# Optimization experiments

Hardware: AMD Instinct MI355X
Metric: run time of the kernel (lower is better)

Reference implementation:

```python
import jax, jax.numpy as jnp
import numpy as np

NUM_VISUAL = 16
MAX_PATCH = 1024
DIM = 1280
NUM_HEADS = 16
HEAD_DIM = DIM // NUM_HEADS  # 80


def _make_rope_cache(key):
    # cos/sin cache per (visual, patch): (N, P, 1, head_dim*2) = [cos | sin]
    inv_freq = 1.0 / (10000.0 ** (jnp.arange(0, HEAD_DIM, 2, dtype=jnp.float32) / HEAD_DIM))  # (hd/2,)
    pos = jnp.arange(MAX_PATCH, dtype=jnp.float32)  # (P,)
    freqs = pos[:, None] * inv_freq[None, :]              # (P, hd/2)
    emb = jnp.concatenate([freqs, freqs], axis=-1)        # (P, hd)
    cos = jnp.cos(emb)
    sin = jnp.sin(emb)
    cache = jnp.concatenate([cos, sin], axis=-1)          # (P, 2*hd)
    return jnp.broadcast_to(cache[None, :, None, :], (NUM_VISUAL, MAX_PATCH, 1, 2 * HEAD_DIM))


def setup_inputs() -> dict:
    key = jax.random.key(0)
    k1, k2, k3, k4, k5, k6 = jax.random.split(key, 6)
    s = 0.02
    hidden_states = jax.random.normal(k1, (NUM_VISUAL, MAX_PATCH, DIM), dtype=jnp.float32)
    rope_cache = _make_rope_cache(k2)
    seq_lens = jax.random.randint(k3, (NUM_VISUAL,), 512, MAX_PATCH + 1, dtype=jnp.int32)
    w_qkv = jax.random.normal(k4, (3 * DIM, DIM), dtype=jnp.float32) * s
    b_qkv = jnp.zeros((3 * DIM,), dtype=jnp.float32)
    w_proj = jax.random.normal(k5, (DIM, DIM), dtype=jnp.float32) * s
    b_proj = jnp.zeros((DIM,), dtype=jnp.float32)
    return {"hidden_states": hidden_states, "rope_cache": rope_cache, "seq_lens": seq_lens,
            "w_qkv": w_qkv, "b_qkv": b_qkv, "w_proj": w_proj, "b_proj": b_proj}


def _rotate_half(x):
    x1, x2 = jnp.split(x, 2, axis=-1)
    return jnp.concatenate([-x2, x1], axis=-1)


def reference(hidden_states, rope_cache, seq_lens, w_qkv, b_qkv, w_proj, b_proj):
    N, P, D = hidden_states.shape
    H, hd = NUM_HEADS, HEAD_DIM
    # QKV projection: (N, P, 3D) -> (N, P, 3, H, hd)
    qkv = (hidden_states @ w_qkv.T + b_qkv).reshape(N, P, 3, H, hd)
    q, k, v = qkv[:, :, 0], qkv[:, :, 1], qkv[:, :, 2]  # each (N, P, H, hd)
    # RoPE via precomputed cos/sin: rope_cache (N, P, 1, 2*hd)
    cos = rope_cache[..., :hd]   # (N, P, 1, hd), broadcasts over heads
    sin = rope_cache[..., hd:]
    q = q * cos + _rotate_half(q) * sin
    k = k * cos + _rotate_half(k) * sin
    # Attention with key-padding mask (BlockMask equivalent for varlen patches)
    scale = 1.0 / jnp.sqrt(jnp.asarray(hd, dtype=q.dtype))
    scores = jnp.einsum("nqhd,nkhd->nhqk", q, k) * scale  # (N, H, P, P)
    key_valid = jnp.arange(P, dtype=jnp.int32)[None, :] < seq_lens[:, None]  # (N, P)
    neg = jnp.asarray(-1e30, dtype=scores.dtype)
    scores = jnp.where(key_valid[:, None, None, :], scores, neg)
    attn = jax.nn.softmax(scores, axis=-1)
    out = jnp.einsum("nhqk,nkhd->nqhd", attn, v).reshape(N, P, D)
    return out @ w_proj.T + b_proj
```

## Files before the change

### kernel.cpp

```cpp
#include <hip/hip_runtime.h>
#include <stdint.h>

#define DIM     1280
#define NHEADS  16
#define HD      80
#define NV      16
#define MAXP    1024
#define MTOT    (NV*MAXP)

typedef __bf16 bf16;
using bf16x8 = __attribute__((ext_vector_type(8))) __bf16;
using bf16x4 = __attribute__((ext_vector_type(4))) __bf16;
using f32x4  = __attribute__((ext_vector_type(4))) float;

#define GLOAD_LDS16(g, l)                                                     \
    __builtin_amdgcn_global_load_lds(                                         \
        (const __attribute__((address_space(1))) void*)(g),                   \
        (__attribute__((address_space(3))) void*)(l), 16, 0, 0)

__global__ __launch_bounds__(256)
void cvt_bf16(const float* __restrict__ src, bf16* __restrict__ dst, int n4)
{
    const int i = blockIdx.x * 256 + threadIdx.x;
    if (i < n4) {
        const float4 f = ((const float4*)src)[i];
        bf16x4 r;
        r[0] = (bf16)f.x; r[1] = (bf16)f.y; r[2] = (bf16)f.z; r[3] = (bf16)f.w;
        ((bf16x4*)dst)[i] = r;
    }
}

template<bool IS_QKV, int NB, int G>
__global__ __launch_bounds__(256)
void gemm_nt_big(const bf16* __restrict__ A, const bf16* __restrict__ B,
                 const float* __restrict__ bias,
                 bf16* __restrict__ out0, bf16* __restrict__ out1,
                 bf16* __restrict__ out2, float* __restrict__ outf)
{
    const int K = DIM;
    __shared__ __align__(16) bf16 SH[2*128*64];
    bf16* const As = SH;
    bf16* const Bs = SH + 128*64;

    const int tid  = threadIdx.x;
    const int lane = tid & 63, wave = tid >> 6;
    const int quad = lane >> 4, c16 = lane & 15;
    const int wm = wave & 1, wn = wave >> 1;

    const int bid = blockIdx.x;
    const int xcd = bid & 7;
    const int idx = bid >> 3;
    const int nbg = idx / (16*G);
    const int rem = idx % (16*G);
    const int mb  = xcd*16 + rem / G;
    const int nb  = nbg*G  + rem % G;

    const int sr   = lane >> 3;
    const int slot = lane & 7;
    const int sc   = (slot ^ sr) * 8;
    const long a_row0 = (long)mb * 128;
    const long b_row0 = (long)nb * 128;

    const bf16* ga[4];
    const bf16* gb[4];
    #pragma unroll
    for (int c = 0; c < 4; ++c) {
        const int seg = c*4 + wave;
        const int row = seg*8 + sr;
        ga[c] = A + (a_row0 + row)*K + sc;
        gb[c] = B + (b_row0 + row)*K + sc;
    }

    f32x4 acc[4][4] = {};
    const int xr = c16 & 7;

    for (int kt = 0; kt < K/64; ++kt) {
        const int k0 = kt * 64;
        __syncthreads();
        #pragma unroll
        for (int c = 0; c < 4; ++c) {
            const int seg = c*4 + wave;
            GLOAD_LDS16(ga[c] + k0, As + seg*512);
            GLOAD_LDS16(gb[c] + k0, Bs + seg*512);
        }
        __syncthreads();
        #pragma unroll
        for (int kk = 0; kk < 2; ++kk) {
            const int j  = kk*4 + quad;
            const int ko = ((j ^ xr) * 8);
            bf16x8 af[4], bfr[4];
            #pragma unroll
            for (int mt = 0; mt < 4; ++mt)
                af[mt] = *(const bf16x8*)(As + (wm*64 + mt*16 + c16)*64 + ko);
            #pragma unroll
            for (int nt = 0; nt < 4; ++nt)
                bfr[nt] = *(const bf16x8*)(Bs + (wn*64 + nt*16 + c16)*64 + ko);
            #pragma unroll
            for (int mt = 0; mt < 4; ++mt)
                #pragma unroll
                for (int nt = 0; nt < 4; ++nt)
                    acc[mt][nt] = __builtin_amdgcn_mfma_f32_16x16x32_bf16(
                        af[mt], bfr[nt], acc[mt][nt], 0, 0, 0);
        }
    }

    if constexpr (IS_QKV) {
        const int which = nb / 10;
        if (which < 2) {
            bf16* const dst = (which == 0) ? out0 : out1;
            #pragma unroll
            for (int nt = 0; nt < 4; ++nt) {
                const int col = nb*128 + wn*64 + nt*16 + c16;
                const float bv = bias[col];
                const int rr = col - which*DIM;
                const int h  = rr / HD;
                const int d  = rr - h*HD;
                #pragma unroll
                for (int mt = 0; mt < 4; ++mt) {
                    #pragma unroll
                    for (int r = 0; r < 4; ++r) {
                        const int row = mb*128 + wm*64 + mt*16 + quad*4 + r;
                        const int n = row >> 10, p = row & 1023;
                        dst[((long)((n*NHEADS + h)*MAXP + p))*HD + d] =
                            (bf16)(acc[mt][nt][r] + bv);
                    }
                }
            }
        } else {
            __syncthreads();
            #pragma unroll
            for (int nt = 0; nt < 4; ++nt) {
                const int dl0 = wn*64 + nt*16 + c16;
                const float bv = bias[nb*128 + dl0];
                const int swz = (dl0 & 15) << 3;
                #pragma unroll
                for (int mt = 0; mt < 4; ++mt) {
                    #pragma unroll
                    for (int r = 0; r < 4; ++r) {
                        const int pl = wm*64 + mt*16 + quad*4 + r;
                        SH[dl0*128 + (pl ^ swz)] = (bf16)(acc[mt][nt][r] + bv);
                    }
                }
            }
            __syncthreads();
            const int n_    = mb >> 3;
            const int pbase = (mb & 7) * 128;
            #pragma unroll
            for (int it = 0; it < 8; ++it) {
                const int c  = tid + 256*it;
                const int dl = c >> 4, j = c & 15;
                const int p0 = (j ^ (dl & 15)) << 3;
                const int rr = (nb - 20)*128 + dl;
                const int hh = rr / HD;
                const int dd = rr - hh*HD;
                bf16x8 v = *(const bf16x8*)(SH + dl*128 + j*8);
                *(bf16x8*)(out2 + ((long)((n_*NHEADS + hh)*HD + dd))*MAXP
                                  + pbase + p0) = v;
            }
        }
    } else {
        #pragma unroll
        for (int nt = 0; nt < 4; ++nt) {
            const int col = nb*128 + wn*64 + nt*16 + c16;
            const float bv = bias[col];
            #pragma unroll
            for (int mt = 0; mt < 4; ++mt) {
                #pragma unroll
                for (int r = 0; r < 4; ++r) {
                    const int row = mb*128 + wm*64 + mt*16 + quad*4 + r;
                    outf[(long)row*DIM + col] = acc[mt][nt][r] + bv;
                }
            }
        }
    }
}

__global__ __launch_bounds__(320)
void rope_kernel(bf16* __restrict__ qb, bf16* __restrict__ kb,
                 const float* __restrict__ rope)
{
    const int tid = threadIdx.x;
    const int j   = tid % 5;
    const int rl  = tid / 5;
    const long grow = (long)blockIdx.x * 64 + rl;
    const int p = (int)(grow & 1023);
    const int h = (int)((grow >> 10) & 15);
    const int n = (int)((grow >> 14) & 15);
    const int a = (int)(grow >> 18);
    bf16* const arr = a ? kb : qb;
    const long base = ((long)((n*NHEADS + h)*MAXP + p))*HD;
    const float* rc = rope + ((long)(n*MAXP + p))*160;
    const int d = j*8;

    bf16x8 x1v = *(const bf16x8*)(arr + base + d);
    bf16x8 x2v = *(const bf16x8*)(arr + base + 40 + d);

    float c1[8], s1[8], c2[8], s2[8];
    *(float4*)(c1)   = *(const float4*)(rc + d);
    *(float4*)(c1+4) = *(const float4*)(rc + d + 4);
    *(float4*)(s1)   = *(const float4*)(rc + 80 + d);
    *(float4*)(s1+4) = *(const float4*)(rc + 80 + d + 4);
    *(float4*)(c2)   = *(const float4*)(rc + 40 + d);
    *(float4*)(c2+4) = *(const float4*)(rc + 40 + d + 4);
    *(float4*)(s2)   = *(const float4*)(rc + 120 + d);
    *(float4*)(s2+4) = *(const float4*)(rc + 120 + d + 4);

    const float QS = 0.11180339887498949f * 1.4426950408889634f;
    bf16x8 r1, r2;
    #pragma unroll
    for (int i = 0; i < 8; ++i) {
        const float x1 = (float)x1v[i];
        const float x2 = (float)x2v[i];
        float o1 = x1 * c1[i] - x2 * s1[i];
        float o2 = x2 * c2[i] + x1 * s2[i];
        if (a == 0) { o1 *= QS; o2 *= QS; }
        r1[i] = (bf16)o1;
        r2[i] = (bf16)o2;
    }
    *(bf16x8*)(arr + base + d)      = r1;
    *(bf16x8*)(arr + base + 40 + d) = r2;
}

__global__ __launch_bounds__(256)
void attn_kernel(const bf16* __restrict__ qb, const bf16* __restrict__ kb,
                 const bf16* __restrict__ vt, const int* __restrict__ seq_lens,
                 bf16* __restrict__ outb)
{
    __shared__ __align__(16) bf16 Qs[64*104];
    __shared__ __align__(16) bf16 Ks[64*104];
    __shared__ __align__(16) bf16 Vts[80*72];

    const int tid  = threadIdx.x;
    const int lane = tid & 63, wave = tid >> 6;
    const int quad = lane >> 4, c16 = lane & 15;
    const int qt = blockIdx.x, h = blockIdx.y, n = blockIdx.z;
    const int seqlen = seq_lens[n];

    const long qkbase = ((long)(n*NHEADS + h)) * MAXP * HD;
    const long vbase  = ((long)(n*NHEADS + h)) * HD * MAXP;

    const float4 zero4 = make_float4(0.f, 0.f, 0.f, 0.f);

    for (int i = tid; i < 768; i += 256) {
        int row = i / 12, c = i % 12;
        float4 v = (c < 10)
            ? *(const float4*)(qb + qkbase + (long)(qt*64 + row)*HD + c*8)
            : zero4;
        *(float4*)(Qs + row*104 + c*8) = v;
    }
    __syncthreads();
    bf16x8 aq[3];
    #pragma unroll
    for (int kc = 0; kc < 3; ++kc)
        aq[kc] = *(const bf16x8*)(Qs + (wave*16 + c16)*104 + kc*32 + quad*8);

    float mrow = -1e30f, lrow = 0.0f;
    f32x4 O[5] = {};

    union U8 { bf16x8 v; bf16x4 h[2]; };

    const int nkt = (seqlen + 63) >> 6;
    for (int kt = 0; kt < nkt; ++kt) {
        __syncthreads();
        for (int i = tid; i < 768; i += 256) {
            int row = i / 12, c = i % 12;
            float4 v = (c < 10)
                ? *(const float4*)(kb + qkbase + (long)(kt*64 + row)*HD + c*8)
                : zero4;
            *(float4*)(Ks + row*104 + c*8) = v;
        }
        for (int i = tid; i < 640; i += 256) {
            int d = i >> 3, c = i & 7;
            *(float4*)(Vts + d*72 + c*8) =
                *(const float4*)(vt + vbase + (long)d*MAXP + kt*64 + c*8);
        }
        __syncthreads();

        f32x4 S[4] = {};
        #pragma unroll
        for (int kc = 0; kc < 3; ++kc) {
            const int ko = kc*32 + quad*8;
            #pragma unroll
            for (int nt = 0; nt < 4; ++nt) {
                bf16x8 ak = *(const bf16x8*)(Ks + (nt*16 + c16)*104 + ko);
                S[nt] = __builtin_amdgcn_mfma_f32_16x16x32_bf16(ak, aq[kc], S[nt], 0,0,0);
            }
        }
        #pragma unroll
        for (int nt = 0; nt < 4; ++nt) {
            const int key0 = kt*64 + nt*16 + quad*4;
            #pragma unroll
            for (int r = 0; r < 4; ++r)
                if (key0 + r >= seqlen) S[nt][r] = -1e30f;
        }

        float mx[4];
        #pragma unroll
        for (int nt = 0; nt < 4; ++nt)
            mx[nt] = fmaxf(fmaxf(S[nt][0], S[nt][1]), fmaxf(S[nt][2], S[nt][3]));
        float pmax = fmaxf(fmaxf(mx[0], mx[1]), fmaxf(mx[2], mx[3]));
        pmax = fmaxf(pmax, __shfl_xor(pmax, 16));
        pmax = fmaxf(pmax, __shfl_xor(pmax, 32));

        const float nm    = fmaxf(mrow, pmax);
        const float alpha = exp2f(mrow - nm);
        mrow = nm;

        #pragma unroll
        for (int nt = 0; nt < 4; ++nt)
            #pragma unroll
            for (int r = 0; r < 4; ++r)
                S[nt][r] = exp2f(S[nt][r] - nm);

        float sm[4];
        #pragma unroll
        for (int nt = 0; nt < 4; ++nt)
            sm[nt] = (S[nt][0] + S[nt][1]) + (S[nt][2] + S[nt][3]);
        float rs = (sm[0] + sm[1]) + (sm[2] + sm[3]);
        rs += __shfl_xor(rs, 16);
        rs += __shfl_xor(rs, 32);
        lrow = lrow * alpha + rs;

        #pragma unroll
        for (int dt = 0; dt < 5; ++dt)
            #pragma unroll
            for (int r = 0; r < 4; ++r)
                O[dt][r] *= alpha;

        bf16x8 Pk[2];
        #pragma unroll
        for (int nt = 0; nt < 4; ++nt)
            #pragma unroll
            for (int r = 0; r < 4; ++r)
                Pk[nt >> 1][(nt & 1)*4 + r] = (bf16)S[nt][r];

        #pragma unroll
        for (int kc = 0; kc < 2; ++kc) {
            #pragma unroll
            for (int dt = 0; dt < 5; ++dt) {
                U8 av;
                av.h[0] = *(const bf16x4*)(Vts + (dt*16 + c16)*72 + kc*32 + quad*4);
                av.h[1] = *(const bf16x4*)(Vts + (dt*16 + c16)*72 + kc*32 + 16 + quad*4);
                O[dt] = __builtin_amdgcn_mfma_f32_16x16x32_bf16(av.v, Pk[kc], O[dt], 0,0,0);
            }
        }
    }

    const float inv = 1.0f / lrow;
    #pragma unroll
    for (int dt = 0; dt < 5; ++dt)
        #pragma unroll
        for (int r = 0; r < 4; ++r)
            Qs[(wave*16 + c16)*104 + dt*16 + quad*4 + r] = (bf16)(O[dt][r] * inv);
    __syncthreads();
    for (int i = tid; i < 640; i += 256) {
        const int row = i / 10, c = i % 10;
        const float4 v = *(const float4*)(Qs + row*104 + c*8);
        *(float4*)(outb + ((long)(n*MAXP + qt*64 + row))*DIM + h*HD + c*8) = v;
    }
}

extern "C" void kernel_launch(void* const* d_in, const int* in_sizes, int n_in,
                              void* d_out, int out_size, void* d_ws, size_t ws_size,
                              hipStream_t stream)
{
    const float* hidden = (const float*)d_in[0];
    const float* rope   = (const float*)d_in[1];
    const int*   seql   = (const int*)d_in[2];
    const float* wqkv   = (const float*)d_in[3];
    const float* bqkv   = (const float*)d_in[4];
    const float* wproj  = (const float*)d_in[5];
    const float* bproj  = (const float*)d_in[6];
    float* out = (float*)d_out;

    const size_t H_ELEMS  = (size_t)MTOT*DIM;
    const size_t WQ_ELEMS = (size_t)3*DIM*DIM;
    const size_t WP_ELEMS = (size_t)DIM*DIM;
    const size_t QK_ELEMS = (size_t)NV*NHEADS*MAXP*HD;

    bf16* h_bf  = (bf16*)d_ws;
    bf16* wq_bf = h_bf  + H_ELEMS;
    bf16* wp_bf = wq_bf + WQ_ELEMS;

    bf16* q_b = (bf16*)d_out;
    bf16* k_b = q_b + QK_ELEMS;
    bf16* v_t = (bf16*)d_in[0];
    bf16* a_b = v_t + QK_ELEMS;

    cvt_bf16<<<(H_ELEMS/4 + 255)/256, 256, 0, stream>>>(hidden, h_bf, H_ELEMS/4);
    cvt_bf16<<<(WQ_ELEMS/4 + 255)/256, 256, 0, stream>>>(wqkv, wq_bf, WQ_ELEMS/4);
    cvt_bf16<<<(WP_ELEMS/4 + 255)/256, 256, 0, stream>>>(wproj, wp_bf, WP_ELEMS/4);

    gemm_nt_big<true, 30, 6><<<3840, 256, 0, stream>>>(
        h_bf, wq_bf, bqkv, q_b, k_b, v_t, nullptr);

    rope_kernel<<<524288/64, 320, 0, stream>>>(q_b, k_b, rope);

    attn_kernel<<<dim3(MAXP/64, NHEADS, NV), 256, 0, stream>>>(
        q_b, k_b, v_t, seql, a_b);

    gemm_nt_big<false, 10, 10><<<1280, 256, 0, stream>>>(
        a_b, wp_bf, bproj, nullptr, nullptr, nullptr, out);
}
```

Measured before the change: 693.8 us.

## Prefetch next K/V tile into registers and skip unneeded softmax rescales

The attention kernel now issues global loads for the next K and V tile into registers right after the barrier, then writes them to LDS at the start of the following iteration, so load latency overlaps with the current tile's MFMA and softmax work. The key-padding mask is applied only on the last tile. The online-softmax rescale of O and l is skipped when every row's new max stays within 8 of the running max, which cuts the exp and multiply work. MFMA sections are wrapped with s_setprio. The costs are higher register pressure from the prefetch buffers, and with lazy rescaling exp values can reach up to 2^8 before normalization, though this stays within bf16 range.

```diff
diff --git a/kernel.cpp b/kernel.cpp
--- a/kernel.cpp
+++ b/kernel.cpp
@@ -241,6 +241,40 @@
 
     const float4 zero4 = make_float4(0.f, 0.f, 0.f, 0.f);
 
+    int krow[3], kcc[3];
+    #pragma unroll
+    for (int j = 0; j < 3; ++j) {
+        const int i = tid + 256*j;
+        krow[j] = i / 12; kcc[j] = i % 12;
+    }
+    const int vd0 = tid >> 3;
+    const int vd1 = (tid + 256) >> 3;
+    const int vd2 = (tid + 512) >> 3;
+    const int vc  = tid & 7;
+    const bool v2ok = tid < 128;
+
+    float4 kreg[3], vreg[3];
+    auto issue = [&](int ktp) {
+        #pragma unroll
+        for (int j = 0; j < 3; ++j)
+            kreg[j] = (kcc[j] < 10)
+                ? *(const float4*)(kb + qkbase + (long)(ktp*64 + krow[j])*HD + kcc[j]*8)
+                : zero4;
+        vreg[0] = *(const float4*)(vt + vbase + (long)vd0*MAXP + ktp*64 + vc*8);
+        vreg[1] = *(const float4*)(vt + vbase + (long)vd1*MAXP + ktp*64 + vc*8);
+        if (v2ok)
+            vreg[2] = *(const float4*)(vt + vbase + (long)vd2*MAXP + ktp*64 + vc*8);
+    };
+    auto commit = [&]() {
+        #pragma unroll
+        for (int j = 0; j < 3; ++j)
+            *(float4*)(Ks + krow[j]*104 + kcc[j]*8) = kreg[j];
+        *(float4*)(Vts + vd0*72 + vc*8) = vreg[0];
+        *(float4*)(Vts + vd1*72 + vc*8) = vreg[1];
+        if (v2ok) *(float4*)(Vts + vd2*72 + vc*8) = vreg[2];
+    };
+
+    issue(0);
     for (int i = tid; i < 768; i += 256) {
         int row = i / 12, c = i % 12;
         float4 v = (c < 10)
@@ -262,21 +296,12 @@
     const int nkt = (seqlen + 63) >> 6;
     for (int kt = 0; kt < nkt; ++kt) {
         __syncthreads();
-        for (int i = tid; i < 768; i += 256) {
-            int row = i / 12, c = i % 12;
-            float4 v = (c < 10)
-                ? *(const float4*)(kb + qkbase + (long)(kt*64 + row)*HD + c*8)
-                : zero4;
-            *(float4*)(Ks + row*104 + c*8) = v;
-        }
-        for (int i = tid; i < 640; i += 256) {
-            int d = i >> 3, c = i & 7;
-            *(float4*)(Vts + d*72 + c*8) =
-                *(const float4*)(vt + vbase + (long)d*MAXP + kt*64 + c*8);
-        }
+        commit();
         __syncthreads();
+        if (kt + 1 < nkt) issue(kt + 1);
 
         f32x4 S[4] = {};
+        __builtin_amdgcn_s_setprio(1);
         #pragma unroll
         for (int kc = 0; kc < 3; ++kc) {
             const int ko = kc*32 + quad*8;
@@ -286,12 +311,16 @@
                 S[nt] = __builtin_amdgcn_mfma_f32_16x16x32_bf16(ak, aq[kc], S[nt], 0,0,0);
             }
         }
-        #pragma unroll
-        for (int nt = 0; nt < 4; ++nt) {
-            const int key0 = kt*64 + nt*16 + quad*4;
-            #pragma unroll
-            for (int r = 0; r < 4; ++r)
-                if (key0 + r >= seqlen) S[nt][r] = -1e30f;
+        __builtin_amdgcn_s_setprio(0);
+
+        if (kt == nkt - 1) {
+            #pragma unroll
+            for (int nt = 0; nt < 4; ++nt) {
+                const int key0 = kt*64 + nt*16 + quad*4;
+                #pragma unroll
+                for (int r = 0; r < 4; ++r)
+                    if (key0 + r >= seqlen) S[nt][r] = -1e30f;
+            }
         }
 
         float mx[4];
@@ -302,15 +331,23 @@
         pmax = fmaxf(pmax, __shfl_xor(pmax, 16));
         pmax = fmaxf(pmax, __shfl_xor(pmax, 32));
 
-        const float nm    = fmaxf(mrow, pmax);
-        const float alpha = exp2f(mrow - nm);
-        mrow = nm;
+        if (!__all(pmax <= mrow + 8.0f)) {
+            const float nm    = fmaxf(mrow, pmax);
+            const float alpha = exp2f(mrow - nm);
+            mrow = nm;
+            lrow *= alpha;
+            #pragma unroll
+            for (int dt = 0; dt < 5; ++dt)
+                #pragma unroll
+                for (int r = 0; r < 4; ++r)
+                    O[dt][r] *= alpha;
+        }
 
         #pragma unroll
         for (int nt = 0; nt < 4; ++nt)
             #pragma unroll
             for (int r = 0; r < 4; ++r)
-                S[nt][r] = exp2f(S[nt][r] - nm);
+                S[nt][r] = exp2f(S[nt][r] - mrow);
 
         float sm[4];
         #pragma unroll
@@ -319,13 +356,7 @@
         float rs = (sm[0] + sm[1]) + (sm[2] + sm[3]);
         rs += __shfl_xor(rs, 16);
         rs += __shfl_xor(rs, 32);
-        lrow = lrow * alpha + rs;
-
-        #pragma unroll
-        for (int dt = 0; dt < 5; ++dt)
-            #pragma unroll
-            for (int r = 0; r < 4; ++r)
-                O[dt][r] *= alpha;
+        lrow += rs;
 
         bf16x8 Pk[2];
         #pragma unroll
@@ -334,6 +365,7 @@
             for (int r = 0; r < 4; ++r)
                 Pk[nt >> 1][(nt & 1)*4 + r] = (bf16)S[nt][r];
 
+        __builtin_amdgcn_s_setprio(1);
         #pragma unroll
         for (int kc = 0; kc < 2; ++kc) {
             #pragma unroll
@@ -344,6 +376,7 @@
                 O[dt] = __builtin_amdgcn_mfma_f32_16x16x32_bf16(av.v, Pk[kc], O[dt], 0,0,0);
             }
         }
+        __builtin_amdgcn_s_setprio(0);
     }
 
     const float inv = 1.0f / lrow;
```

After: 890.6 us. 1.28x slower.

## Prefetch next K/V tile into registers and add lazy softmax rescaling

Applied to the files above, without the earlier changes.

The attention loop now loads the next K and V tiles from global memory into registers while the current tile is being computed, then writes them to LDS at the start of the next iteration, so global load latency overlaps with MFMA work. The key-padding mask is applied only on the last key tile. The online-softmax rescale of O and l is skipped unless some row's max has grown by more than 8 (log2 units). MFMA sections are also wrapped in s_setprio. This raises register pressure, and lazy rescaling lets exponent values grow up to 2^8 before renormalising.

```diff
diff --git a/kernel.cpp b/kernel.cpp
--- a/kernel.cpp
+++ b/kernel.cpp
@@ -221,6 +221,26 @@
     *(bf16x8*)(arr + base + 40 + d) = r2;
 }
 
+#define ATTN_ISSUE(ktp) do {                                                  \
+    const long kro_ = qkbase + (long)(ktp)*64*HD;                             \
+    kA = k0v ? *(const float4*)(kb + kro_ + (long)kr0*HD + kc0) : zero4;      \
+    kB = k1v ? *(const float4*)(kb + kro_ + (long)kr1*HD + kc1) : zero4;      \
+    kC = k2v ? *(const float4*)(kb + kro_ + (long)kr2*HD + kc2) : zero4;      \
+    const long vro_ = vbase + (long)(ktp)*64 + vc8;                           \
+    vA = *(const float4*)(vt + vro_ + (long)vd0*MAXP);                        \
+    vB = *(const float4*)(vt + vro_ + (long)vd1*MAXP);                        \
+    if (v2ok) vC = *(const float4*)(vt + vro_ + (long)vd2*MAXP);              \
+} while (0)
+
+#define ATTN_COMMIT() do {                                                    \
+    *(float4*)(Ks + kr0*104 + kc0) = kA;                                      \
+    *(float4*)(Ks + kr1*104 + kc1) = kB;                                      \
+    *(float4*)(Ks + kr2*104 + kc2) = kC;                                      \
+    *(float4*)(Vts + vd0*72 + vc8) = vA;                                      \
+    *(float4*)(Vts + vd1*72 + vc8) = vB;                                      \
+    if (v2ok) *(float4*)(Vts + vd2*72 + vc8) = vC;                            \
+} while (0)
+
 __global__ __launch_bounds__(256)
 void attn_kernel(const bf16* __restrict__ qb, const bf16* __restrict__ kb,
                  const bf16* __restrict__ vt, const int* __restrict__ seq_lens,
@@ -241,6 +261,17 @@
 
     const float4 zero4 = make_float4(0.f, 0.f, 0.f, 0.f);
 
+    const int kr0 = tid / 12,         kc0 = (tid % 12) * 8;
+    const int kr1 = (tid + 256) / 12, kc1 = ((tid + 256) % 12) * 8;
+    const int kr2 = (tid + 512) / 12, kc2 = ((tid + 512) % 12) * 8;
+    const bool k0v = kc0 < 80, k1v = kc1 < 80, k2v = kc2 < 80;
+    const int vd0 = tid >> 3, vd1 = vd0 + 32, vd2 = vd0 + 64;
+    const int vc8 = (tid & 7) * 8;
+    const bool v2ok = tid < 128;
+
+    float4 kA, kB, kC, vA, vB, vC;
+
+    ATTN_ISSUE(0);
     for (int i = tid; i < 768; i += 256) {
         int row = i / 12, c = i % 12;
         float4 v = (c < 10)
@@ -262,21 +293,12 @@
     const int nkt = (seqlen + 63) >> 6;
     for (int kt = 0; kt < nkt; ++kt) {
         __syncthreads();
-        for (int i = tid; i < 768; i += 256) {
-            int row = i / 12, c = i % 12;
-            float4 v = (c < 10)
-                ? *(const float4*)(kb + qkbase + (long)(kt*64 + row)*HD + c*8)
-                : zero4;
-            *(float4*)(Ks + row*104 + c*8) = v;
-        }
-        for (int i = tid; i < 640; i += 256) {
-            int d = i >> 3, c = i & 7;
-            *(float4*)(Vts + d*72 + c*8) =
-                *(const float4*)(vt + vbase + (long)d*MAXP + kt*64 + c*8);
-        }
+        ATTN_COMMIT();
         __syncthreads();
+        if (kt + 1 < nkt) ATTN_ISSUE(kt + 1);
 
         f32x4 S[4] = {};
+        __builtin_amdgcn_s_setprio(1);
         #pragma unroll
         for (int kc = 0; kc < 3; ++kc) {
             const int ko = kc*32 + quad*8;
@@ -286,12 +308,16 @@
                 S[nt] = __builtin_amdgcn_mfma_f32_16x16x32_bf16(ak, aq[kc], S[nt], 0,0,0);
             }
         }
-        #pragma unroll
-        for (int nt = 0; nt < 4; ++nt) {
-            const int key0 = kt*64 + nt*16 + quad*4;
-            #pragma unroll
-            for (int r = 0; r < 4; ++r)
-                if (key0 + r >= seqlen) S[nt][r] = -1e30f;
+        __builtin_amdgcn_s_setprio(0);
+
+        if (kt == nkt - 1) {
+            #pragma unroll
+            for (int nt = 0; nt < 4; ++nt) {
+                const int key0 = kt*64 + nt*16 + quad*4;
+                #pragma unroll
+                for (int r = 0; r < 4; ++r)
+                    if (key0 + r >= seqlen) S[nt][r] = -1e30f;
+            }
         }
 
         float mx[4];
@@ -302,15 +328,23 @@
         pmax = fmaxf(pmax, __shfl_xor(pmax, 16));
         pmax = fmaxf(pmax, __shfl_xor(pmax, 32));
 
-        const float nm    = fmaxf(mrow, pmax);
-        const float alpha = exp2f(mrow - nm);
-        mrow = nm;
+        if (!__all(pmax <= mrow + 8.0f)) {
+            const float nm    = fmaxf(mrow, pmax);
+            const float alpha = exp2f(mrow - nm);
+            mrow = nm;
+            lrow *= alpha;
+            #pragma unroll
+            for (int dt = 0; dt < 5; ++dt)
+                #pragma unroll
+                for (int r = 0; r < 4; ++r)
+                    O[dt][r] *= alpha;
+        }
 
         #pragma unroll
         for (int nt = 0; nt < 4; ++nt)
             #pragma unroll
             for (int r = 0; r < 4; ++r)
-                S[nt][r] = exp2f(S[nt][r] - nm);
+                S[nt][r] = exp2f(S[nt][r] - mrow);
 
         float sm[4];
         #pragma unroll
@@ -319,13 +353,7 @@
         float rs = (sm[0] + sm[1]) + (sm[2] + sm[3]);
         rs += __shfl_xor(rs, 16);
         rs += __shfl_xor(rs, 32);
-        lrow = lrow * alpha + rs;
-
-        #pragma unroll
-        for (int dt = 0; dt < 5; ++dt)
-            #pragma unroll
-            for (int r = 0; r < 4; ++r)
-                O[dt][r] *= alpha;
+        lrow += rs;
 
         bf16x8 Pk[2];
         #pragma unroll
@@ -334,6 +362,7 @@
             for (int r = 0; r < 4; ++r)
                 Pk[nt >> 1][(nt & 1)*4 + r] = (bf16)S[nt][r];
 
+        __builtin_amdgcn_s_setprio(1);
         #pragma unroll
         for (int kc = 0; kc < 2; ++kc) {
             #pragma unroll
@@ -344,6 +373,7 @@
                 O[dt] = __builtin_amdgcn_mfma_f32_16x16x32_bf16(av.v, Pk[kc], O[dt], 0,0,0);
             }
         }
+        __builtin_amdgcn_s_setprio(0);
     }
 
     const float inv = 1.0f / lrow;
```

Measured after the change: 657.2 us. 1.06x faster.
